# Kernel tuning notes

Hardware: AMD Instinct MI355X
Metric: run time of the kernel (lower is better)

## Reference

```python
import jax, jax.numpy as jnp
import numpy as np

TEMPERATURE = 1.0
ALPHA = 0.5


def setup_inputs() -> dict:
    key = jax.random.key(0)
    k1, k2, k3 = jax.random.split(key, 3)
    bs, d = 4096, 1024
    return {
        "zi": jax.random.normal(k1, (bs, d), dtype=jnp.float32),
        "zj": jax.random.normal(k2, (bs, d), dtype=jnp.float32),
        "z_orig": jax.random.normal(k3, (bs, d), dtype=jnp.float32),
    }


def _off_diag(M):
    # rows of M with the diagonal removed -> [n, n-1], row-major order,
    # matching torch boolean-mask indexing M[mask].reshape(n, -1)
    n = M.shape[0]
    return M.reshape(-1)[:-1].reshape(n - 1, n + 1)[:, 1:].reshape(n, n - 1)


def _l2norm(x):
    return x / jnp.linalg.norm(x, axis=-1, keepdims=True)


def reference(zi, zj, z_orig):
    bs = zi.shape[0]
    zi_n = _l2norm(zi)
    zj_n = _l2norm(zj)
    zo_n = _l2norm(z_orig)

    logits_ii = (zi_n @ zi_n.T) / TEMPERATURE  # [bs, bs]
    logits_ij = (zi_n @ zj_n.T) / TEMPERATURE
    logits_ji = (zj_n @ zi_n.T) / TEMPERATURE
    logits_jj = (zj_n @ zj_n.T) / TEMPERATURE

    # positives: diagonal entries (logits[~mask] with mask = ones minus diag)
    pos = jnp.concatenate([jnp.diagonal(logits_ij), jnp.diagonal(logits_ji)], axis=0)[:, None]  # [2bs, 1]
    # negatives: off-diagonal entries, [bs, bs-1] each
    neg_i = jnp.concatenate([_off_diag(logits_ii), _off_diag(logits_ij)], axis=1)  # [bs, 2bs-2]
    neg_j = jnp.concatenate([_off_diag(logits_ji), _off_diag(logits_jj)], axis=1)
    neg = jnp.concatenate([neg_i, neg_j], axis=0)  # [2bs, 2bs-2]

    logits = jnp.concatenate([pos, neg], axis=1)  # [2bs, 2bs-1]
    # cross entropy with labels == 0 for every row
    lse = jax.nn.logsumexp(logits, axis=-1)
    contrastive_loss = jnp.mean(lse - logits[:, 0])

    # KL term: softmax / log_softmax over the length-bs diagonal vectors
    logits_io = (zi_n @ zo_n.T) / TEMPERATURE
    logits_jo = (zj_n @ zo_n.T) / TEMPERATURE
    probs_io = jax.nn.softmax(jnp.diagonal(logits_io), axis=-1)          # probs (as in original)
    probs_jo = jax.nn.log_softmax(jnp.diagonal(logits_jo), axis=-1)     # log-probs (target)
    # F.kl_div(input, target, log_target=True, reduction='sum')
    #   = sum(exp(target) * (target - input))
    kl_div_loss = jnp.sum(jnp.exp(probs_jo) * (probs_jo - probs_io))

    return contrastive_loss + ALPHA * kl_div_loss
```

## Files before the change

kernel.cpp:

```cpp
#include <hip/hip_runtime.h>
#include <hip/hip_fp8.h>

typedef int   i32x4  __attribute__((ext_vector_type(4)));
typedef float f32x16 __attribute__((ext_vector_type(16)));

#define BS 4096
#define D 1024
#define M2 8192

#define BK 64
#define NKT (D / BK)
#define NT 64
#define NBLK (NT * (NT + 1) / 2)

#define OFF_Z      ((size_t)0)
#define OFF_SUMEXP ((size_t)M2 * D * 2)
#define OFF_POS    (OFF_SUMEXP + (size_t)M2 * 4)
#define OFF_DIO    (OFF_POS + (size_t)M2 * 4)
#define OFF_DJO    (OFF_DIO + (size_t)BS * 4)

static __device__ __forceinline__ void gload_lds16(const void* g, void* l) {
  __builtin_amdgcn_global_load_lds(
      (__attribute__((address_space(1))) void*)(uintptr_t)g,
      (__attribute__((address_space(3))) void*)(unsigned int)(uintptr_t)l,
      16, 0, 0);
}

__global__ __launch_bounds__(256) void prep_kernel(
    const float* __restrict__ zi, const float* __restrict__ zj,
    const float* __restrict__ zo, unsigned char* __restrict__ Z,
    float* __restrict__ dio, float* __restrict__ djo,
    float* __restrict__ sumexp) {
  const int r = blockIdx.x;
  const int tid = threadIdx.x;
  if (tid < 2) sumexp[2 * r + tid] = 0.f;
  const float4 vi = ((const float4*)(zi + (size_t)r * D))[tid];
  const float4 vj = ((const float4*)(zj + (size_t)r * D))[tid];
  const float4 vo = ((const float4*)(zo + (size_t)r * D))[tid];

  float s[5];
  s[0] = vi.x * vi.x + vi.y * vi.y + vi.z * vi.z + vi.w * vi.w;
  s[1] = vj.x * vj.x + vj.y * vj.y + vj.z * vj.z + vj.w * vj.w;
  s[2] = vo.x * vo.x + vo.y * vo.y + vo.z * vo.z + vo.w * vo.w;
  s[3] = vi.x * vo.x + vi.y * vo.y + vi.z * vo.z + vi.w * vo.w;
  s[4] = vj.x * vo.x + vj.y * vo.y + vj.z * vo.z + vj.w * vo.w;

#pragma unroll
  for (int k = 0; k < 5; ++k)
#pragma unroll
    for (int o = 32; o; o >>= 1) s[k] += __shfl_xor(s[k], o);

  __shared__ float red[4][5];
  const int w = tid >> 6, lane = tid & 63;
  if (lane == 0) {
#pragma unroll
    for (int k = 0; k < 5; ++k) red[w][k] = s[k];
  }
  __syncthreads();
  float tot[5];
#pragma unroll
  for (int k = 0; k < 5; ++k)
    tot[k] = red[0][k] + red[1][k] + red[2][k] + red[3][k];

  const float rsi = 1.0f / sqrtf(tot[0]);
  const float rsj = 1.0f / sqrtf(tot[1]);
  const float rso = 1.0f / sqrtf(tot[2]);

  uchar4 oi, oj;
  oi.x = __hip_fp8_e4m3(vi.x * rsi).__x;
  oi.y = __hip_fp8_e4m3(vi.y * rsi).__x;
  oi.z = __hip_fp8_e4m3(vi.z * rsi).__x;
  oi.w = __hip_fp8_e4m3(vi.w * rsi).__x;
  oj.x = __hip_fp8_e4m3(vj.x * rsj).__x;
  oj.y = __hip_fp8_e4m3(vj.y * rsj).__x;
  oj.z = __hip_fp8_e4m3(vj.z * rsj).__x;
  oj.w = __hip_fp8_e4m3(vj.w * rsj).__x;
  ((uchar4*)(Z + (size_t)r * D))[tid] = oi;
  ((uchar4*)(Z + (size_t)(BS + r) * D))[tid] = oj;

  if (tid == 0) {
    dio[r] = tot[3] * rsi * rso;
    djo[r] = tot[4] * rsj * rso;
  }
}

__global__ __launch_bounds__(256) void gemm_lse_kernel(
    const unsigned char* __restrict__ Z,
    float* __restrict__ sumexp, float* __restrict__ pos) {
  __shared__ __align__(16) unsigned char lA[4][128 * BK];
  __shared__ __align__(16) unsigned char lB[4][128 * BK];
  __shared__ float psumR[2][128];
  __shared__ float psumC[2][128];

  const int torig = blockIdx.x;
  const int t = (torig & 7) * (NBLK / 8) + (torig >> 3);

  int bm = (int)((129.0f - sqrtf(16641.0f - 8.0f * (float)t)) * 0.5f);
  while ((bm + 1) * (129 - (bm + 1)) / 2 <= t) ++bm;
  while (bm * (129 - bm) / 2 > t) --bm;
  const int bn = bm + (t - bm * (129 - bm) / 2);
  const bool isDiag = (bm == bn);

  const int tid = threadIdx.x;
  const int lane = tid & 63, w = tid >> 6;
  const int wr = w >> 1, wc = w & 1;
  const int l31 = lane & 31, lh = lane >> 5;

  const int srow = tid >> 2;
  const int schunk = (tid & 3) ^ ((srow >> 1) & 3);
  const unsigned char* gA = Z + (size_t)(bm * 128 + srow) * D + schunk * 16;
  const unsigned char* gB = Z + (size_t)(bn * 128 + srow) * D + schunk * 16;

#define STAGE(buf)                                                \
  do {                                                            \
    gload_lds16(gA, &lA[buf][tid * 16]);                          \
    gload_lds16(gA + (size_t)64 * D, &lA[buf][tid * 16 + 4096]);  \
    gload_lds16(gB, &lB[buf][tid * 16]);                          \
    gload_lds16(gB + (size_t)64 * D, &lB[buf][tid * 16 + 4096]);  \
    gA += BK; gB += BK;                                           \
  } while (0)

  int offA[2][2], offB[2][2];
#pragma unroll
  for (int mi = 0; mi < 2; ++mi) {
    const int rowA = wr * 64 + mi * 32 + l31;
    const int rowB = wc * 64 + mi * 32 + l31;
    const int keyA = (rowA >> 1) & 3, keyB = (rowB >> 1) & 3;
#pragma unroll
    for (int c = 0; c < 2; ++c) {
      offA[mi][c] = rowA * BK + ((lh * 2 + c) ^ keyA) * 16;
      offB[mi][c] = rowB * BK + ((lh * 2 + c) ^ keyB) * 16;
    }
  }

  f32x16 acc00 = {}, acc01 = {}, acc10 = {}, acc11 = {};

  STAGE(0);
  STAGE(1);

  for (int kt = 0; kt < NKT; ++kt) {
    const int cur = kt & 3;
    if (kt < NKT - 2) {
      STAGE((kt + 2) & 3);
      asm volatile("s_waitcnt vmcnt(8)");
    } else if (kt == NKT - 2) {
      asm volatile("s_waitcnt vmcnt(4)");
    } else {
      asm volatile("s_waitcnt vmcnt(0)");
    }
    __builtin_amdgcn_s_barrier();
    __builtin_amdgcn_sched_barrier(0);

    const unsigned char* Ab = &lA[cur][0];
    const unsigned char* Bb = &lB[cur][0];
    union { i32x4 v; long l[2]; } ra0, ra1, rb0, rb1;
    long aS[2][4], bS[2][4];
#pragma unroll
    for (int mi = 0; mi < 2; ++mi) {
      ra0.v = *(const i32x4*)(Ab + offA[mi][0]);
      ra1.v = *(const i32x4*)(Ab + offA[mi][1]);
      aS[mi][0] = ra0.l[0]; aS[mi][1] = ra0.l[1];
      aS[mi][2] = ra1.l[0]; aS[mi][3] = ra1.l[1];
    }
#pragma unroll
    for (int ni = 0; ni < 2; ++ni) {
      rb0.v = *(const i32x4*)(Bb + offB[ni][0]);
      rb1.v = *(const i32x4*)(Bb + offB[ni][1]);
      bS[ni][0] = rb0.l[0]; bS[ni][1] = rb0.l[1];
      bS[ni][2] = rb1.l[0]; bS[ni][3] = rb1.l[1];
    }

    __builtin_amdgcn_s_setprio(1);
#pragma unroll
    for (int s = 0; s < 4; ++s) {
      acc00 = __builtin_amdgcn_mfma_f32_32x32x16_fp8_fp8(aS[0][s], bS[0][s], acc00, 0, 0, 0);
      acc01 = __builtin_amdgcn_mfma_f32_32x32x16_fp8_fp8(aS[0][s], bS[1][s], acc01, 0, 0, 0);
      acc10 = __builtin_amdgcn_mfma_f32_32x32x16_fp8_fp8(aS[1][s], bS[0][s], acc10, 0, 0, 0);
      acc11 = __builtin_amdgcn_mfma_f32_32x32x16_fp8_fp8(aS[1][s], bS[1][s], acc11, 0, 0, 0);
    }
    __builtin_amdgcn_s_setprio(0);
  }
#undef STAGE

  const int brow = bm * 128, bcol = bn * 128;
  float cs[2] = {0.f, 0.f};
#pragma unroll
  for (int mi = 0; mi < 2; ++mi) {
#pragma unroll
    for (int r = 0; r < 16; ++r) {
      const int rit = (r & 3) + 8 * (r >> 2) + 4 * lh;
      const int gq = brow + wr * 64 + mi * 32 + rit;
      const int prt = gq ^ BS;
      float sse = 0.f;
#pragma unroll
      for (int ni = 0; ni < 2; ++ni) {
        const int gc = bcol + wc * 64 + ni * 32 + l31;
        const float v = (mi == 0) ? ((ni == 0) ? acc00[r] : acc01[r])
                                  : ((ni == 0) ? acc10[r] : acc11[r]);
        if (gc == prt) { pos[gq] = v; pos[gc] = v; }
        const float e = (gc != gq) ? __expf(v) : 0.f;
        sse += e;
        cs[ni] += e;
      }
      sse += __shfl_xor(sse, 1);
      sse += __shfl_xor(sse, 2);
      sse += __shfl_xor(sse, 4);
      sse += __shfl_xor(sse, 8);
      sse += __shfl_xor(sse, 16);
      if (l31 == 0) psumR[wc][wr * 64 + mi * 32 + rit] = sse;
    }
  }
  if (!isDiag) {
#pragma unroll
    for (int ni = 0; ni < 2; ++ni) {
      cs[ni] += __shfl_xor(cs[ni], 32);
      if (lh == 0) psumC[wr][wc * 64 + ni * 32 + l31] = cs[ni];
    }
  }
  __syncthreads();
  if (tid < 128) atomicAdd(&sumexp[brow + tid], psumR[0][tid] + psumR[1][tid]);
  if (!isDiag && tid < 128)
    atomicAdd(&sumexp[bcol + tid], psumC[0][tid] + psumC[1][tid]);
}

__global__ __launch_bounds__(256) void finalize_kernel(
    const float* __restrict__ sumexp, const float* __restrict__ pos,
    const float* __restrict__ dio, const float* __restrict__ djo,
    float* __restrict__ out) {
  const int tid = threadIdx.x;
  float s1 = 0.f, sa = 0.f, sb = 0.f;
  for (int q = tid; q < M2; q += 256) s1 += __logf(sumexp[q]) - pos[q];
  for (int r = tid; r < BS; r += 256) { sa += __expf(dio[r]); sb += __expf(djo[r]); }

  __shared__ float red[4][3];
  float v3[3] = {s1, sa, sb};
#pragma unroll
  for (int k = 0; k < 3; ++k)
#pragma unroll
    for (int o = 32; o; o >>= 1) v3[k] += __shfl_xor(v3[k], o);
  const int w = tid >> 6, lane = tid & 63;
  if (lane == 0) { red[w][0] = v3[0]; red[w][1] = v3[1]; red[w][2] = v3[2]; }
  __syncthreads();
  const float S1 = red[0][0] + red[1][0] + red[2][0] + red[3][0];
  const float A  = red[0][1] + red[1][1] + red[2][1] + red[3][1];
  const float B  = red[0][2] + red[1][2] + red[2][2] + red[3][2];
  const float logB = __logf(B);
  const float invA = 1.0f / A;

  float kl = 0.f;
  for (int r = tid; r < BS; r += 256) {
    const float lp = djo[r] - logB;
    kl += __expf(lp) * (lp - __expf(dio[r]) * invA);
  }
#pragma unroll
  for (int o = 32; o; o >>= 1) kl += __shfl_xor(kl, o);
  __shared__ float red2[4];
  if (lane == 0) red2[w] = kl;
  __syncthreads();
  if (tid == 0) {
    const float KL = red2[0] + red2[1] + red2[2] + red2[3];
    out[0] = S1 / (float)M2 + 0.5f * KL;
  }
}

extern "C" void kernel_launch(void* const* d_in, const int* in_sizes, int n_in,
                              void* d_out, int out_size, void* d_ws, size_t ws_size,
                              hipStream_t stream) {
  const float* zi = (const float*)d_in[0];
  const float* zj = (const float*)d_in[1];
  const float* zo = (const float*)d_in[2];
  char* ws = (char*)d_ws;
  unsigned char* Z = (unsigned char*)(ws + OFF_Z);
  float* sumexp = (float*)(ws + OFF_SUMEXP);
  float* pos    = (float*)(ws + OFF_POS);
  float* dio    = (float*)(ws + OFF_DIO);
  float* djo    = (float*)(ws + OFF_DJO);

  prep_kernel<<<BS, 256, 0, stream>>>(zi, zj, zo, Z, dio, djo, sumexp);
  gemm_lse_kernel<<<NBLK, 256, 0, stream>>>(Z, sumexp, pos);
  finalize_kernel<<<1, 256, 0, stream>>>(sumexp, pos, dio, djo, (float*)d_out);
}
```

Before: 121.3 us.

## Enlarge GEMM tiles to 256x256 with 8 waves and phased LDS pipeline

Moves the symmetric fp8 GEMM+LSE kernel from 128x128 tiles with 4 waves to 256x256 tiles with 8 waves (2x4 layout, each wave computing 128x64). Global-to-LDS staging now uses a double buffer and is split into four quarter loads interleaved with four MFMA phases, each separated by barriers. The aim is more data reuse per byte loaded and better overlap of loads with compute. In exchange there are fewer blocks (528 vs 2080), which causes load imbalance across CUs, plus more barriers per k-step and higher register use.

```diff
diff --git a/kernel.cpp b/kernel.cpp
--- a/kernel.cpp
+++ b/kernel.cpp
@@ -8,10 +8,10 @@
 #define D 1024
 #define M2 8192
 
-#define BK 64
-#define NKT (D / BK)
-#define NT 64
-#define NBLK (NT * (NT + 1) / 2)
+#define BKB 64
+#define NKT 16
+#define NT2 32
+#define NBLK2 528
 
 #define OFF_Z      ((size_t)0)
 #define OFF_SUMEXP ((size_t)M2 * D * 2)
@@ -84,143 +84,222 @@
   }
 }
 
-__global__ __launch_bounds__(256) void gemm_lse_kernel(
+__global__ __launch_bounds__(512, 2) void gemm_lse_kernel(
     const unsigned char* __restrict__ Z,
     float* __restrict__ sumexp, float* __restrict__ pos) {
-  __shared__ __align__(16) unsigned char lA[4][128 * BK];
-  __shared__ __align__(16) unsigned char lB[4][128 * BK];
-  __shared__ float psumR[2][128];
-  __shared__ float psumC[2][128];
+  __shared__ __align__(16) unsigned char lA[2][256 * BKB];
+  __shared__ __align__(16) unsigned char lB[2][256 * BKB];
+  __shared__ float psumR[4][256];
+  __shared__ float psumC[2][256];
 
   const int torig = blockIdx.x;
-  const int t = (torig & 7) * (NBLK / 8) + (torig >> 3);
-
-  int bm = (int)((129.0f - sqrtf(16641.0f - 8.0f * (float)t)) * 0.5f);
-  while ((bm + 1) * (129 - (bm + 1)) / 2 <= t) ++bm;
-  while (bm * (129 - bm) / 2 > t) --bm;
-  const int bn = bm + (t - bm * (129 - bm) / 2);
+  const int t = (torig & 7) * (NBLK2 / 8) + (torig >> 3);
+
+  int bm = 0;
+  while ((bm + 1) * (65 - (bm + 1)) / 2 <= t) ++bm;
+  const int bn = bm + (t - bm * (65 - bm) / 2);
   const bool isDiag = (bm == bn);
 
   const int tid = threadIdx.x;
   const int lane = tid & 63, w = tid >> 6;
-  const int wr = w >> 1, wc = w & 1;
+  const int wr = w >> 2, wc = w & 3;
   const int l31 = lane & 31, lh = lane >> 5;
 
-  const int srow = tid >> 2;
-  const int schunk = (tid & 3) ^ ((srow >> 1) & 3);
-  const unsigned char* gA = Z + (size_t)(bm * 128 + srow) * D + schunk * 16;
-  const unsigned char* gB = Z + (size_t)(bn * 128 + srow) * D + schunk * 16;
-
-#define STAGE(buf)                                                \
-  do {                                                            \
-    gload_lds16(gA, &lA[buf][tid * 16]);                          \
-    gload_lds16(gA + (size_t)64 * D, &lA[buf][tid * 16 + 4096]);  \
-    gload_lds16(gB, &lB[buf][tid * 16]);                          \
-    gload_lds16(gB + (size_t)64 * D, &lB[buf][tid * 16 + 4096]);  \
-    gA += BK; gB += BK;                                           \
+  const int rIdx = tid >> 2;
+  const int rAa = rIdx + ((tid >= 256) ? 64 : 0);
+  const int rAb = rAa + 64;
+  const int rBa = (rIdx & 31) + (tid >> 7) * 64;
+  const int rBb = rBa + 32;
+  const int dAa = tid * 16 + ((tid >= 256) ? 4096 : 0);
+  const int dAb = dAa + 4096;
+  const int dBa = tid * 16 + (tid >> 7) * 2048;
+  const int dBb = dBa + 2048;
+  const unsigned char* pAa = Z + (size_t)(bm * 256 + rAa) * D + ((tid & 3) ^ ((rAa >> 1) & 3)) * 16;
+  const unsigned char* pAb = Z + (size_t)(bm * 256 + rAb) * D + ((tid & 3) ^ ((rAb >> 1) & 3)) * 16;
+  const unsigned char* pBa = Z + (size_t)(bn * 256 + rBa) * D + ((tid & 3) ^ ((rBa >> 1) & 3)) * 16;
+  const unsigned char* pBb = Z + (size_t)(bn * 256 + rBb) * D + ((tid & 3) ^ ((rBb >> 1) & 3)) * 16;
+
+#define ST_AA(buf) do { gload_lds16(pAa, &lA[buf][dAa]); pAa += BKB; } while (0)
+#define ST_AB(buf) do { gload_lds16(pAb, &lA[buf][dAb]); pAb += BKB; } while (0)
+#define ST_BA(buf) do { gload_lds16(pBa, &lB[buf][dBa]); pBa += BKB; } while (0)
+#define ST_BB(buf) do { gload_lds16(pBb, &lB[buf][dBb]); pBb += BKB; } while (0)
+
+  int offA[4][2], offB[2][2];
+#pragma unroll
+  for (int mi = 0; mi < 4; ++mi) {
+    const int rA = wr * 128 + mi * 32 + l31;
+    const int key = (rA >> 1) & 3;
+    offA[mi][0] = rA * BKB + ((lh * 2) ^ key) * 16;
+    offA[mi][1] = rA * BKB + ((lh * 2 + 1) ^ key) * 16;
+  }
+#pragma unroll
+  for (int ni = 0; ni < 2; ++ni) {
+    const int rB = wc * 64 + ni * 32 + l31;
+    const int key = (rB >> 1) & 3;
+    offB[ni][0] = rB * BKB + ((lh * 2) ^ key) * 16;
+    offB[ni][1] = rB * BKB + ((lh * 2 + 1) ^ key) * 16;
+  }
+
+  union U { i32x4 v; long l[2]; };
+  f32x16 c00 = {}, c01 = {}, c10 = {}, c11 = {};
+  f32x16 c20 = {}, c21 = {}, c30 = {}, c31 = {};
+
+#define SBAR() __builtin_amdgcn_sched_barrier(0)
+#define BAR()  __builtin_amdgcn_s_barrier()
+
+#define MFMA8(cL, cH, a0, a1, b0, b1)                                              \
+  do {                                                                             \
+    cL = __builtin_amdgcn_mfma_f32_32x32x16_fp8_fp8(a0.l[0], b0.l[0], cL, 0,0,0);  \
+    cH = __builtin_amdgcn_mfma_f32_32x32x16_fp8_fp8(a1.l[0], b0.l[0], cH, 0,0,0);  \
+    cL = __builtin_amdgcn_mfma_f32_32x32x16_fp8_fp8(a0.l[1], b0.l[1], cL, 0,0,0);  \
+    cH = __builtin_amdgcn_mfma_f32_32x32x16_fp8_fp8(a1.l[1], b0.l[1], cH, 0,0,0);  \
+    cL = __builtin_amdgcn_mfma_f32_32x32x16_fp8_fp8(a0.l[2], b1.l[0], cL, 0,0,0);  \
+    cH = __builtin_amdgcn_mfma_f32_32x32x16_fp8_fp8(a1.l[2], b1.l[0], cH, 0,0,0);  \
+    cL = __builtin_amdgcn_mfma_f32_32x32x16_fp8_fp8(a0.l[3], b1.l[1], cL, 0,0,0);  \
+    cH = __builtin_amdgcn_mfma_f32_32x32x16_fp8_fp8(a1.l[3], b1.l[1], cH, 0,0,0);  \
   } while (0)
 
-  int offA[2][2], offB[2][2];
-#pragma unroll
-  for (int mi = 0; mi < 2; ++mi) {
-    const int rowA = wr * 64 + mi * 32 + l31;
-    const int rowB = wc * 64 + mi * 32 + l31;
-    const int keyA = (rowA >> 1) & 3, keyB = (rowB >> 1) & 3;
-#pragma unroll
-    for (int c = 0; c < 2; ++c) {
-      offA[mi][c] = rowA * BK + ((lh * 2 + c) ^ keyA) * 16;
-      offB[mi][c] = rowB * BK + ((lh * 2 + c) ^ keyB) * 16;
-    }
-  }
-
-  f32x16 acc00 = {}, acc01 = {}, acc10 = {}, acc11 = {};
-
-  STAGE(0);
-  STAGE(1);
+  struct A4 { long l[4]; };
+
+  ST_AA(0); ST_BA(0); ST_AB(0); ST_BB(0);
+  asm volatile("s_waitcnt vmcnt(2)");
+  BAR(); SBAR();
 
   for (int kt = 0; kt < NKT; ++kt) {
-    const int cur = kt & 3;
-    if (kt < NKT - 2) {
-      STAGE((kt + 2) & 3);
-      asm volatile("s_waitcnt vmcnt(8)");
-    } else if (kt == NKT - 2) {
-      asm volatile("s_waitcnt vmcnt(4)");
-    } else {
-      asm volatile("s_waitcnt vmcnt(0)");
-    }
-    __builtin_amdgcn_s_barrier();
-    __builtin_amdgcn_sched_barrier(0);
-
-    const unsigned char* Ab = &lA[cur][0];
-    const unsigned char* Bb = &lB[cur][0];
-    union { i32x4 v; long l[2]; } ra0, ra1, rb0, rb1;
-    long aS[2][4], bS[2][4];
-#pragma unroll
-    for (int mi = 0; mi < 2; ++mi) {
-      ra0.v = *(const i32x4*)(Ab + offA[mi][0]);
-      ra1.v = *(const i32x4*)(Ab + offA[mi][1]);
-      aS[mi][0] = ra0.l[0]; aS[mi][1] = ra0.l[1];
-      aS[mi][2] = ra1.l[0]; aS[mi][3] = ra1.l[1];
-    }
-#pragma unroll
-    for (int ni = 0; ni < 2; ++ni) {
-      rb0.v = *(const i32x4*)(Bb + offB[ni][0]);
-      rb1.v = *(const i32x4*)(Bb + offB[ni][1]);
-      bS[ni][0] = rb0.l[0]; bS[ni][1] = rb0.l[1];
-      bS[ni][2] = rb1.l[0]; bS[ni][3] = rb1.l[1];
-    }
-
+    const int cur = kt & 1, nxt = cur ^ 1;
+    const unsigned char* Abase = &lA[cur][0];
+    const unsigned char* Bbase = &lB[cur][0];
+    const bool more = (kt + 1 < NKT);
+
+    A4 a0, a1; U b0, b1, tmp0, tmp1;
+
+    tmp0.v = *(const i32x4*)(Abase + offA[0][0]); tmp1.v = *(const i32x4*)(Abase + offA[0][1]);
+    a0.l[0] = tmp0.l[0]; a0.l[1] = tmp0.l[1]; a0.l[2] = tmp1.l[0]; a0.l[3] = tmp1.l[1];
+    tmp0.v = *(const i32x4*)(Abase + offA[1][0]); tmp1.v = *(const i32x4*)(Abase + offA[1][1]);
+    a1.l[0] = tmp0.l[0]; a1.l[1] = tmp0.l[1]; a1.l[2] = tmp1.l[0]; a1.l[3] = tmp1.l[1];
+    b0.v = *(const i32x4*)(Bbase + offB[0][0]); b1.v = *(const i32x4*)(Bbase + offB[0][1]);
+    if (more) ST_AA(nxt);
+    SBAR(); BAR();
     __builtin_amdgcn_s_setprio(1);
-#pragma unroll
-    for (int s = 0; s < 4; ++s) {
-      acc00 = __builtin_amdgcn_mfma_f32_32x32x16_fp8_fp8(aS[0][s], bS[0][s], acc00, 0, 0, 0);
-      acc01 = __builtin_amdgcn_mfma_f32_32x32x16_fp8_fp8(aS[0][s], bS[1][s], acc01, 0, 0, 0);
-      acc10 = __builtin_amdgcn_mfma_f32_32x32x16_fp8_fp8(aS[1][s], bS[0][s], acc10, 0, 0, 0);
-      acc11 = __builtin_amdgcn_mfma_f32_32x32x16_fp8_fp8(aS[1][s], bS[1][s], acc11, 0, 0, 0);
+    {
+      U a0lo, a0hi, a1lo, a1hi;
+      a0lo.l[0] = a0.l[0]; a0lo.l[1] = a0.l[1]; a0hi.l[0] = a0.l[2]; a0hi.l[1] = a0.l[3];
+      a1lo.l[0] = a1.l[0]; a1lo.l[1] = a1.l[1]; a1hi.l[0] = a1.l[2]; a1hi.l[1] = a1.l[3];
+      c00 = __builtin_amdgcn_mfma_f32_32x32x16_fp8_fp8(a0.l[0], b0.l[0], c00, 0,0,0);
+      c10 = __builtin_amdgcn_mfma_f32_32x32x16_fp8_fp8(a1.l[0], b0.l[0], c10, 0,0,0);
+      c00 = __builtin_amdgcn_mfma_f32_32x32x16_fp8_fp8(a0.l[1], b0.l[1], c00, 0,0,0);
+      c10 = __builtin_amdgcn_mfma_f32_32x32x16_fp8_fp8(a1.l[1], b0.l[1], c10, 0,0,0);
+      c00 = __builtin_amdgcn_mfma_f32_32x32x16_fp8_fp8(a0.l[2], b1.l[0], c00, 0,0,0);
+      c10 = __builtin_amdgcn_mfma_f32_32x32x16_fp8_fp8(a1.l[2], b1.l[0], c10, 0,0,0);
+      c00 = __builtin_amdgcn_mfma_f32_32x32x16_fp8_fp8(a0.l[3], b1.l[1], c00, 0,0,0);
+      c10 = __builtin_amdgcn_mfma_f32_32x32x16_fp8_fp8(a1.l[3], b1.l[1], c10, 0,0,0);
     }
     __builtin_amdgcn_s_setprio(0);
-  }
-#undef STAGE
-
-  const int brow = bm * 128, bcol = bn * 128;
-  float cs[2] = {0.f, 0.f};
-#pragma unroll
-  for (int mi = 0; mi < 2; ++mi) {
+    SBAR();
+    if (more) asm volatile("s_waitcnt vmcnt(1)");
+    else      asm volatile("s_waitcnt vmcnt(0)");
+    BAR(); SBAR();
+
+    b0.v = *(const i32x4*)(Bbase + offB[1][0]); b1.v = *(const i32x4*)(Bbase + offB[1][1]);
+    if (more) ST_BA(nxt);
+    SBAR(); BAR();
+    __builtin_amdgcn_s_setprio(1);
+    c01 = __builtin_amdgcn_mfma_f32_32x32x16_fp8_fp8(a0.l[0], b0.l[0], c01, 0,0,0);
+    c11 = __builtin_amdgcn_mfma_f32_32x32x16_fp8_fp8(a1.l[0], b0.l[0], c11, 0,0,0);
+    c01 = __builtin_amdgcn_mfma_f32_32x32x16_fp8_fp8(a0.l[1], b0.l[1], c01, 0,0,0);
+    c11 = __builtin_amdgcn_mfma_f32_32x32x16_fp8_fp8(a1.l[1], b0.l[1], c11, 0,0,0);
+    c01 = __builtin_amdgcn_mfma_f32_32x32x16_fp8_fp8(a0.l[2], b1.l[0], c01, 0,0,0);
+    c11 = __builtin_amdgcn_mfma_f32_32x32x16_fp8_fp8(a1.l[2], b1.l[0], c11, 0,0,0);
+    c01 = __builtin_amdgcn_mfma_f32_32x32x16_fp8_fp8(a0.l[3], b1.l[1], c01, 0,0,0);
+    c11 = __builtin_amdgcn_mfma_f32_32x32x16_fp8_fp8(a1.l[3], b1.l[1], c11, 0,0,0);
+    __builtin_amdgcn_s_setprio(0);
+    SBAR(); BAR(); SBAR();
+
+    tmp0.v = *(const i32x4*)(Abase + offA[2][0]); tmp1.v = *(const i32x4*)(Abase + offA[2][1]);
+    a0.l[0] = tmp0.l[0]; a0.l[1] = tmp0.l[1]; a0.l[2] = tmp1.l[0]; a0.l[3] = tmp1.l[1];
+    tmp0.v = *(const i32x4*)(Abase + offA[3][0]); tmp1.v = *(const i32x4*)(Abase + offA[3][1]);
+    a1.l[0] = tmp0.l[0]; a1.l[1] = tmp0.l[1]; a1.l[2] = tmp1.l[0]; a1.l[3] = tmp1.l[1];
+    b0.v = *(const i32x4*)(Bbase + offB[0][0]); b1.v = *(const i32x4*)(Bbase + offB[0][1]);
+    if (more) ST_AB(nxt);
+    SBAR(); BAR();
+    __builtin_amdgcn_s_setprio(1);
+    c20 = __builtin_amdgcn_mfma_f32_32x32x16_fp8_fp8(a0.l[0], b0.l[0], c20, 0,0,0);
+    c30 = __builtin_amdgcn_mfma_f32_32x32x16_fp8_fp8(a1.l[0], b0.l[0], c30, 0,0,0);
+    c20 = __builtin_amdgcn_mfma_f32_32x32x16_fp8_fp8(a0.l[1], b0.l[1], c20, 0,0,0);
+    c30 = __builtin_amdgcn_mfma_f32_32x32x16_fp8_fp8(a1.l[1], b0.l[1], c30, 0,0,0);
+    c20 = __builtin_amdgcn_mfma_f32_32x32x16_fp8_fp8(a0.l[2], b1.l[0], c20, 0,0,0);
+    c30 = __builtin_amdgcn_mfma_f32_32x32x16_fp8_fp8(a1.l[2], b1.l[0], c30, 0,0,0);
+    c20 = __builtin_amdgcn_mfma_f32_32x32x16_fp8_fp8(a0.l[3], b1.l[1], c20, 0,0,0);
+    c30 = __builtin_amdgcn_mfma_f32_32x32x16_fp8_fp8(a1.l[3], b1.l[1], c30, 0,0,0);
+    __builtin_amdgcn_s_setprio(0);
+    SBAR(); BAR(); SBAR();
+
+    b0.v = *(const i32x4*)(Bbase + offB[1][0]); b1.v = *(const i32x4*)(Bbase + offB[1][1]);
+    if (more) ST_BB(nxt);
+    SBAR(); BAR();
+    __builtin_amdgcn_s_setprio(1);
+    c21 = __builtin_amdgcn_mfma_f32_32x32x16_fp8_fp8(a0.l[0], b0.l[0], c21, 0,0,0);
+    c31 = __builtin_amdgcn_mfma_f32_32x32x16_fp8_fp8(a1.l[0], b0.l[0], c31, 0,0,0);
+    c21 = __builtin_amdgcn_mfma_f32_32x32x16_fp8_fp8(a0.l[1], b0.l[1], c21, 0,0,0);
+    c31 = __builtin_amdgcn_mfma_f32_32x32x16_fp8_fp8(a1.l[1], b0.l[1], c31, 0,0,0);
+    c21 = __builtin_amdgcn_mfma_f32_32x32x16_fp8_fp8(a0.l[2], b1.l[0], c21, 0,0,0);
+    c31 = __builtin_amdgcn_mfma_f32_32x32x16_fp8_fp8(a1.l[2], b1.l[0], c31, 0,0,0);
+    c21 = __builtin_amdgcn_mfma_f32_32x32x16_fp8_fp8(a0.l[3], b1.l[1], c21, 0,0,0);
+    c31 = __builtin_amdgcn_mfma_f32_32x32x16_fp8_fp8(a1.l[3], b1.l[1], c31, 0,0,0);
+    __builtin_amdgcn_s_setprio(0);
+    SBAR();
+    if (more) { asm volatile("s_waitcnt vmcnt(2)"); }
+    BAR(); SBAR();
+  }
+#undef ST_AA
+#undef ST_AB
+#undef ST_BA
+#undef ST_BB
+
+  const int brow = bm * 256, bcol = bn * 256;
+  float cs0 = 0.f, cs1 = 0.f;
+#pragma unroll
+  for (int mi = 0; mi < 4; ++mi) {
 #pragma unroll
     for (int r = 0; r < 16; ++r) {
       const int rit = (r & 3) + 8 * (r >> 2) + 4 * lh;
-      const int gq = brow + wr * 64 + mi * 32 + rit;
+      const int gq = brow + wr * 128 + mi * 32 + rit;
       const int prt = gq ^ BS;
       float sse = 0.f;
 #pragma unroll
       for (int ni = 0; ni < 2; ++ni) {
         const int gc = bcol + wc * 64 + ni * 32 + l31;
-        const float v = (mi == 0) ? ((ni == 0) ? acc00[r] : acc01[r])
-                                  : ((ni == 0) ? acc10[r] : acc11[r]);
+        const float v =
+            (mi == 0) ? (ni == 0 ? c00[r] : c01[r]) :
+            (mi == 1) ? (ni == 0 ? c10[r] : c11[r]) :
+            (mi == 2) ? (ni == 0 ? c20[r] : c21[r]) :
+                        (ni == 0 ? c30[r] : c31[r]);
         if (gc == prt) { pos[gq] = v; pos[gc] = v; }
         const float e = (gc != gq) ? __expf(v) : 0.f;
         sse += e;
-        cs[ni] += e;
+        if (ni == 0) cs0 += e; else cs1 += e;
       }
       sse += __shfl_xor(sse, 1);
       sse += __shfl_xor(sse, 2);
       sse += __shfl_xor(sse, 4);
       sse += __shfl_xor(sse, 8);
       sse += __shfl_xor(sse, 16);
-      if (l31 == 0) psumR[wc][wr * 64 + mi * 32 + rit] = sse;
+      if (l31 == 0) psumR[wc][wr * 128 + mi * 32 + rit] = sse;
     }
   }
-  if (!isDiag) {
-#pragma unroll
-    for (int ni = 0; ni < 2; ++ni) {
-      cs[ni] += __shfl_xor(cs[ni], 32);
-      if (lh == 0) psumC[wr][wc * 64 + ni * 32 + l31] = cs[ni];
-    }
+  cs0 += __shfl_xor(cs0, 32);
+  cs1 += __shfl_xor(cs1, 32);
+  if (lh == 0) {
+    psumC[wr][wc * 64 + l31] = cs0;
+    psumC[wr][wc * 64 + 32 + l31] = cs1;
   }
   __syncthreads();
-  if (tid < 128) atomicAdd(&sumexp[brow + tid], psumR[0][tid] + psumR[1][tid]);
-  if (!isDiag && tid < 128)
-    atomicAdd(&sumexp[bcol + tid], psumC[0][tid] + psumC[1][tid]);
+  if (tid < 256) {
+    atomicAdd(&sumexp[brow + tid],
+              psumR[0][tid] + psumR[1][tid] + psumR[2][tid] + psumR[3][tid]);
+    if (!isDiag)
+      atomicAdd(&sumexp[bcol + tid], psumC[0][tid] + psumC[1][tid]);
+  }
 }
 
 __global__ __launch_bounds__(256) void finalize_kernel(
@@ -277,6 +356,6 @@
   float* djo    = (float*)(ws + OFF_DJO);
 
   prep_kernel<<<BS, 256, 0, stream>>>(zi, zj, zo, Z, dio, djo, sumexp);
-  gemm_lse_kernel<<<NBLK, 256, 0, stream>>>(Z, sumexp, pos);
+  gemm_lse_kernel<<<NBLK2, 512, 0, stream>>>(Z, sumexp, pos);
   finalize_kernel<<<1, 256, 0, stream>>>(sumexp, pos, dio, djo, (float*)d_out);
 }
```

Result: slower. 148.5 us (+22.4%).
